# Performance work log

Measured on AMD Instinct MI355X. Metric: run time of the kernel, lower is better.

The kernel has to match this reference:

```python
import jax, jax.numpy as jnp
import numpy as np
from jax import lax

B, T, D_IN = 16, 512, 128
H_ENC, D_LAT, H_CTX, H_PRED = 512, 256, 512, 512
K_STEPS, TEMP = 12, 0.1


def setup_inputs() -> dict:
    ks = jax.random.split(jax.random.key(0), 8)
    def w(i, fi, fo):
        return jax.random.normal(ks[i], (fi, fo), jnp.float32) * (1.0 / float(np.sqrt(fi)))
    return {
        "x": jax.random.normal(ks[0], (B, T, D_IN), jnp.float32),
        "enc_w1": w(1, D_IN, H_ENC), "enc_b1": jnp.zeros((H_ENC,), jnp.float32),
        "enc_w2": w(2, H_ENC, H_ENC), "enc_b2": jnp.zeros((H_ENC,), jnp.float32),
        "enc_w3": w(3, H_ENC, D_LAT), "enc_b3": jnp.zeros((D_LAT,), jnp.float32),
        "gru_wi": w(4, D_LAT, 3 * H_CTX), "gru_bi": jnp.zeros((3 * H_CTX,), jnp.float32),
        "gru_wh": w(5, H_CTX, 3 * H_CTX), "gru_bhn": jnp.zeros((H_CTX,), jnp.float32),
        "pred_w1": w(6, H_CTX, H_PRED), "pred_b1": jnp.zeros((H_PRED,), jnp.float32),
        "pred_w2": w(7, H_PRED, D_LAT), "pred_b2": jnp.zeros((D_LAT,), jnp.float32),
    }


def _gru(z, gru_wi, gru_bi, gru_wh, gru_bhn):
    # flax GRUCell: r=sig(Wir x + bir + Whr h); u=sig(Wiz x + biz + Whz h);
    Bsz = z.shape[0]
    H = gru_wh.shape[0]
    xi = z @ gru_wi + gru_bi          # [B, T, 3H] precomputed input projections
    xi = jnp.swapaxes(xi, 0, 1)       # [T, B, 3H]

    def step(h, x_t):
        hp = h @ gru_wh               # [B, 3H]
        xr, xu, xn = jnp.split(x_t, 3, axis=-1)
        hr, hu, hn = jnp.split(hp, 3, axis=-1)
        r = jax.nn.sigmoid(xr + hr)
        u = jax.nn.sigmoid(xu + hu)
        n = jnp.tanh(xn + r * (hn + gru_bhn))
        h_new = (1.0 - u) * n + u * h
        return h_new, h_new

    h0 = jnp.zeros((Bsz, H), z.dtype)
    _, outs = lax.scan(step, h0, xi)  # [T, B, H]
    return jnp.swapaxes(outs, 0, 1)   # [B, T, H]


def reference(x, enc_w1, enc_b1, enc_w2, enc_b2, enc_w3, enc_b3,
              gru_wi, gru_bi, gru_wh, gru_bhn,
              pred_w1, pred_b1, pred_w2, pred_b2):
    # Encoder MLP
    h = jax.nn.relu(x @ enc_w1 + enc_b1)
    h = jax.nn.relu(h @ enc_w2 + enc_b2)
    z = h @ enc_w3 + enc_b3                         # [B, T, D_LAT]
    # GRU context network
    c = _gru(z, gru_wi, gru_bi, gru_wh, gru_bhn)    # [B, T, H_CTX]
    # InfoNCE loss (prediction net is identical across k, so hoist it)
    c_t = c[:, :-K_STEPS, :].reshape(-1, c.shape[-1])   # [N, H_CTX], N=B*(T-K)
    p = jax.nn.relu(c_t @ pred_w1 + pred_b1) @ pred_w2 + pred_b2
    p = p / jnp.linalg.norm(p, axis=1, keepdims=True)   # [N, D_LAT]
    total = jnp.zeros((), z.dtype)
    for k in range(1, K_STEPS + 1):
        zt = z[:, k:T - K_STEPS + k, :].reshape(-1, z.shape[-1])
        zt = zt / jnp.linalg.norm(zt, axis=1, keepdims=True)
        sim = (p @ zt.T) / TEMP                         # [N, N]
        # -mean(diag(log_softmax)) = -mean(diag(sim) - logsumexp(sim, axis=1))
        total = total + (-jnp.mean(jnp.diagonal(sim) - jax.nn.logsumexp(sim, axis=1)))
    loss = total / K_STEPS
    return z, c, loss
```

## Files before the change

### kernel.cpp

```cpp
#include <hip/hip_runtime.h>
#include <cstdint>
#include <cstddef>

typedef unsigned short u16;
typedef unsigned int   u32;
typedef unsigned long long u64;
typedef __attribute__((ext_vector_type(8))) short bf16x8;
typedef __attribute__((ext_vector_type(4))) float f32x4;
typedef __attribute__((ext_vector_type(4))) unsigned int u32x4;

typedef __attribute__((address_space(1))) const unsigned int as1c_uint;
typedef __attribute__((address_space(3))) unsigned int as3_uint;

__device__ __forceinline__ void async16(const void* g, void* l) {
  __builtin_amdgcn_global_load_lds((as1c_uint*)g, (as3_uint*)l, 16, 0, 0);
}
__device__ __forceinline__ float bf2f(u16 u) {
  return __uint_as_float(((u32)u) << 16);
}
__device__ __forceinline__ u16 f2bf(float x) {
  u32 u = __float_as_uint(x);
  u32 r = u + 0x7FFFu + ((u >> 16) & 1u);
  return (u16)(r >> 16);
}

__device__ __forceinline__ void bar_lds() {
  asm volatile("s_waitcnt lgkmcnt(0)" ::: "memory");
  __builtin_amdgcn_s_barrier();
  asm volatile("" ::: "memory");
}

__device__ __forceinline__ u32 ld_u32_ic(const void* p) {
  u32 v;
  asm volatile("global_load_dword %0, %1, off sc0 sc1\n\ts_waitcnt vmcnt(0)"
               : "=v"(v) : "v"(p) : "memory");
  return v;
}
__device__ __forceinline__ void st_u32_ic(void* p, u32 v) {
  asm volatile("global_store_dword %0, %1, off sc0 sc1" :: "v"(p), "v"(v) : "memory");
}
__device__ __forceinline__ void ld_h64_ic(const void* p, u32x4& a, u32x4& b,
                                          u32x4& c, u32x4& d) {
  asm volatile(
      "global_load_dwordx4 %0, %4, off sc0 sc1\n\t"
      "global_load_dwordx4 %1, %4, off offset:16 sc0 sc1\n\t"
      "global_load_dwordx4 %2, %4, off offset:32 sc0 sc1\n\t"
      "global_load_dwordx4 %3, %4, off offset:48 sc0 sc1\n\t"
      "s_waitcnt vmcnt(0)"
      : "=&v"(a), "=&v"(b), "=&v"(c), "=&v"(d) : "v"(p) : "memory");
}

__global__ void cvt_k(const float4* __restrict__ in, ushort4* __restrict__ out) {
  int i = blockIdx.x * 256 + threadIdx.x;
  float4 v = in[i];
  ushort4 o;
  o.x = f2bf(v.x); o.y = f2bf(v.y); o.z = f2bf(v.z); o.w = f2bf(v.w);
  out[i] = o;
}

__global__ void tr_k(const float* __restrict__ in, u16* __restrict__ out, int K, int N) {
  __shared__ u16 t[32][33];
  int bn = blockIdx.x * 32, bk = blockIdx.y * 32;
  int x = threadIdx.x, y = threadIdx.y;
#pragma unroll
  for (int i = 0; i < 32; i += 8)
    t[y + i][x] = f2bf(in[(size_t)(bk + y + i) * N + bn + x]);
  __syncthreads();
#pragma unroll
  for (int i = 0; i < 32; i += 8)
    out[(size_t)(bn + y + i) * K + bk + x] = t[x][y + i];
}

__global__ __launch_bounds__(256) void gemm_k(
    const u16* __restrict__ A, const u16* __restrict__ Bt,
    const float* __restrict__ bias, u16* __restrict__ Cbf, float* __restrict__ Cf,
    int N, int K, int act) {
  __shared__ __align__(16) u16 As[128 * 32];
  __shared__ __align__(16) u16 Bs[128 * 32];
  int tid = threadIdx.x;
  int lane = tid & 63, w = tid >> 6;
  int wm = w >> 1, wn = w & 1;
  int mm = lane & 15, kh = lane >> 4;
  int m0 = blockIdx.y * 128, n0 = blockIdx.x * 128;

  f32x4 zero = {0.f, 0.f, 0.f, 0.f};
  f32x4 acc[4][4];
#pragma unroll
  for (int i = 0; i < 4; ++i)
#pragma unroll
    for (int j = 0; j < 4; ++j) acc[i][j] = zero;

  for (int kt = 0; kt < K; kt += 32) {
#pragma unroll
    for (int it = 0; it < 2; ++it) {
      int q = tid + it * 256;
      int row = q >> 2, kc = (q & 3) * 8;
      async16(A  + (size_t)(m0 + row) * K + kt + kc, &As[q * 8]);
      async16(Bt + (size_t)(n0 + row) * K + kt + kc, &Bs[q * 8]);
    }
    __syncthreads();
    bf16x8 av[4], bv[4];
#pragma unroll
    for (int i = 0; i < 4; ++i) {
      av[i] = *(const bf16x8*)&As[(wm * 64 + i * 16 + mm) * 32 + kh * 8];
      bv[i] = *(const bf16x8*)&Bs[(wn * 64 + i * 16 + mm) * 32 + kh * 8];
    }
#pragma unroll
    for (int im = 0; im < 4; ++im)
#pragma unroll
      for (int in = 0; in < 4; ++in)
        acc[im][in] = __builtin_amdgcn_mfma_f32_16x16x32_bf16(av[im], bv[in], acc[im][in], 0, 0, 0);
    __syncthreads();
  }

#pragma unroll
  for (int im = 0; im < 4; ++im)
#pragma unroll
    for (int in = 0; in < 4; ++in)
#pragma unroll
      for (int r = 0; r < 4; ++r) {
        int gm = m0 + wm * 64 + im * 16 + kh * 4 + r;
        int gn = n0 + wn * 64 + in * 16 + mm;
        float v = acc[im][in][r] + bias[gn];
        if (act) v = fmaxf(v, 0.f);
        size_t off = (size_t)gm * N + gn;
        if (Cbf) Cbf[off] = f2bf(v);
        if (Cf)  Cf[off]  = v;
      }
}

__global__ __launch_bounds__(256) void norm_k(const u16* __restrict__ in,
                                              u16* __restrict__ out, int pack) {
  int row = blockIdx.x * 4 + (threadIdx.x >> 6);
  int lane = threadIdx.x & 63;
  ushort4 v = ((const ushort4*)(in + (size_t)row * 256))[lane];
  float a = bf2f(v.x), b = bf2f(v.y), c = bf2f(v.z), d = bf2f(v.w);
  float s = a * a + b * b + c * c + d * d;
#pragma unroll
  for (int o = 32; o; o >>= 1) s += __shfl_xor(s, o);
  float rn = rsqrtf(s);
  int orow = row;
  if (pack) {
    int bb = row >> 9, tt = row & 511;
    if (tt >= 500) return;
    orow = bb * 500 + tt;
  }
  ushort4 o4;
  o4.x = f2bf(a * rn); o4.y = f2bf(b * rn);
  o4.z = f2bf(c * rn); o4.w = f2bf(d * rn);
  *(ushort4*)(out + (size_t)orow * 256 + lane * 4) = o4;
}

#define HS 520

__global__ __launch_bounds__(512, 1) void gru_k(
    const u16* __restrict__ xi, const float* __restrict__ WH,
    const float* __restrict__ BHN, float* __restrict__ cf,
    u16* __restrict__ cbf, u16* hbuf, u32* flags) {
  __shared__ __align__(16) u16 hs[16 * HS];
  __shared__ float xis[2 * 1536];
  __shared__ float gts[1536];
  __shared__ float hnf[512];

  int tid = threadIdx.x;
  int role = blockIdx.x;
  int c0 = role * 32;

  int lane = tid & 63, w = tid >> 6;
  int mm = lane & 15, kh = lane >> 4;

  bf16x8 wf[16];
  if (w < 6) {
    int gcol = (w >> 1) * 512 + c0 + (w & 1) * 16 + mm;
    int kb = kh * 8;
#pragma unroll
    for (int kk = 0; kk < 16; ++kk) {
      bf16x8 tf;
#pragma unroll
      for (int j = 0; j < 8; ++j)
        tf[j] = (short)f2bf(WH[(size_t)(kk * 32 + kb + j) * 1536 + gcol]);
      wf[kk] = tf;
    }
  }
  int cr = tid >> 4, cj = (tid & 15) * 2;
  float bhn0 = 0.f, bhn1 = 0.f;
  if (w < 4) { bhn0 = BHN[c0 + cj]; bhn1 = BHN[c0 + cj + 1]; }

  int tt = tid - 384;
  size_t xoff[12];
  u16 xpre[12];
  if (w >= 6) {
#pragma unroll
    for (int j = 0; j < 12; ++j) {
      int v = j * 128 + tt;
      int b = v / 96, q = v - b * 96;
      int gcol = (q >> 5) * 512 + c0 + (q & 31);
      xoff[j] = (size_t)b * 512 * 1536 + gcol;
      xis[v] = bf2f(xi[xoff[j]]);
    }
#pragma unroll
    for (int j = 0; j < 12; ++j) xpre[j] = xi[xoff[j] + 1536];
  }

  for (int t = 0; t < 512; ++t) {
    if (w < 4) {
      if (t == 0) {
        for (int i = tid; i < 16 * HS; i += 256) hs[i] = 0;
      } else {
        int iter = 0;
        const u32* fl = &flags[tid & 15];
        while (ld_u32_ic(fl) < (u32)t) { if (++iter > (1 << 20)) break; }
        const u16* hb = hbuf + (size_t)(t & 1) * 8192 + (tid >> 4) * 512 + (tid & 15) * 32;
        u32x4 a, b, c, d;
        ld_h64_ic(hb, a, b, c, d);
        u32x4* dst = (u32x4*)&hs[(tid >> 4) * HS + (tid & 15) * 32];
        dst[0] = a; dst[1] = b; dst[2] = c; dst[3] = d;
      }
    } else if (w >= 6) {
      if (t > 0) {
        int v = tt * 4;
        int b = v >> 5, col = v & 31;
        size_t co = ((size_t)b * 512 + (t - 1)) * 512 + c0 + col;
        float4 o;
        o.x = hnf[v]; o.y = hnf[v + 1]; o.z = hnf[v + 2]; o.w = hnf[v + 3];
        *(float4*)&cf[co] = o;
        uint2 pk;
        pk.x = (u32)f2bf(o.x) | ((u32)f2bf(o.y) << 16);
        pk.y = (u32)f2bf(o.z) | ((u32)f2bf(o.w) << 16);
        *(uint2*)&cbf[co] = pk;
      }
      if (t < 511) {
        float* xd = &xis[((t + 1) & 1) * 1536];
#pragma unroll
        for (int j = 0; j < 12; ++j) xd[j * 128 + tt] = bf2f(xpre[j]);
      }
      if (t < 510) {
        const u16* xs = xi + (size_t)(t + 2) * 1536;
#pragma unroll
        for (int j = 0; j < 12; ++j) xpre[j] = xs[xoff[j]];
      }
    }
    bar_lds();

    if (w < 6) {
      f32x4 acc = {0.f, 0.f, 0.f, 0.f};
#pragma unroll
      for (int kk = 0; kk < 16; ++kk) {
        bf16x8 a = *(const bf16x8*)&hs[mm * HS + kk * 32 + kh * 8];
        acc = __builtin_amdgcn_mfma_f32_16x16x32_bf16(a, wf[kk], acc, 0, 0, 0);
      }
      int gc = (w >> 1) * 32 + (w & 1) * 16 + mm;
#pragma unroll
      for (int r = 0; r < 4; ++r) gts[(kh * 4 + r) * 96 + gc] = acc[r];
    }
    bar_lds();

    if (w < 4) {
      const float* xc = &xis[(t & 1) * 1536] + cr * 96;
      const float* gr_ = &gts[cr * 96];
      float hp0 = bf2f(hs[cr * HS + c0 + cj]);
      float hp1 = bf2f(hs[cr * HS + c0 + cj + 1]);
      float r0 = 1.f / (1.f + __expf(-(xc[cj] + gr_[cj])));
      float u0 = 1.f / (1.f + __expf(-(xc[32 + cj] + gr_[32 + cj])));
      float nx0 = xc[64 + cj] + r0 * (gr_[64 + cj] + bhn0);
      float n0 = 1.f - 2.f / (__expf(2.f * nx0) + 1.f);
      float h0 = (1.f - u0) * n0 + u0 * hp0;
      float r1 = 1.f / (1.f + __expf(-(xc[cj + 1] + gr_[cj + 1])));
      float u1 = 1.f / (1.f + __expf(-(xc[33 + cj] + gr_[33 + cj])));
      float nx1 = xc[65 + cj] + r1 * (gr_[65 + cj] + bhn1);
      float n1 = 1.f - 2.f / (__expf(2.f * nx1) + 1.f);
      float h1v = (1.f - u1) * n1 + u1 * hp1;
      hnf[cr * 32 + cj] = h0;
      hnf[cr * 32 + cj + 1] = h1v;
      u32 pk = (u32)f2bf(h0) | ((u32)f2bf(h1v) << 16);
      st_u32_ic(hbuf + (size_t)((t + 1) & 1) * 8192 + cr * 512 + c0 + cj, pk);
      asm volatile("s_waitcnt vmcnt(0)" ::: "memory");
    }
    bar_lds();
    if (tid == 0) st_u32_ic(&flags[role], (u32)(t + 1));
  }

  if (w >= 6) {
    int v = tt * 4;
    int b = v >> 5, col = v & 31;
    size_t co = ((size_t)b * 512 + 511) * 512 + c0 + col;
    float4 o;
    o.x = hnf[v]; o.y = hnf[v + 1]; o.z = hnf[v + 2]; o.w = hnf[v + 3];
    *(float4*)&cf[co] = o;
    uint2 pk;
    pk.x = (u32)f2bf(o.x) | ((u32)f2bf(o.y) << 16);
    pk.y = (u32)f2bf(o.z) | ((u32)f2bf(o.w) << 16);
    *(uint2*)&cbf[co] = pk;
  }
}

__global__ __launch_bounds__(256) void sgemm_k(
    const u16* __restrict__ P, const u16* __restrict__ Z,
    float* __restrict__ g, float* __restrict__ diag) {
  __shared__ __align__(16) u16 Ap[128 * 256];
  __shared__ __align__(16) u16 Bs[128 * 32];
  __shared__ float gacc[128 * 128];
  int tid = threadIdx.x;
  int lane = tid & 63, w = tid >> 6;
  int wm = w >> 1, wn = w & 1;
  int mm = lane & 15, kh = lane >> 4;
  int r0 = blockIdx.y * 128, t0 = blockIdx.x * 128;

#pragma unroll
  for (int it = 0; it < 16; ++it) {
    int q = tid + it * 256;
    int row = q >> 5, kc = (q & 31) * 8;
    async16(P + (size_t)(r0 + row) * 256 + kc, &Ap[q * 8]);
  }
  for (int i = tid; i < 128 * 128; i += 256) gacc[i] = 0.f;
  __syncthreads();

  f32x4 zero = {0.f, 0.f, 0.f, 0.f};
  for (int b = 0; b < 16; ++b) {
    int n0 = b * 512 + t0;
    f32x4 acc[4][4];
#pragma unroll
    for (int i = 0; i < 4; ++i)
#pragma unroll
      for (int j = 0; j < 4; ++j) acc[i][j] = zero;

    for (int kk = 0; kk < 8; ++kk) {
#pragma unroll
      for (int it = 0; it < 2; ++it) {
        int q = tid + it * 256;
        int row = q >> 2, kc = (q & 3) * 8;
        async16(Z + (size_t)(n0 + row) * 256 + kk * 32 + kc, &Bs[q * 8]);
      }
      __syncthreads();
      bf16x8 av[4], bv[4];
#pragma unroll
      for (int i = 0; i < 4; ++i) {
        av[i] = *(const bf16x8*)&Ap[(wm * 64 + i * 16 + mm) * 256 + kk * 32 + kh * 8];
        bv[i] = *(const bf16x8*)&Bs[(wn * 64 + i * 16 + mm) * 32 + kh * 8];
      }
#pragma unroll
      for (int im = 0; im < 4; ++im)
#pragma unroll
        for (int in = 0; in < 4; ++in)
          acc[im][in] = __builtin_amdgcn_mfma_f32_16x16x32_bf16(av[im], bv[in], acc[im][in], 0, 0, 0);
      __syncthreads();
    }
#pragma unroll
    for (int im = 0; im < 4; ++im)
#pragma unroll
      for (int in = 0; in < 4; ++in)
#pragma unroll
        for (int r = 0; r < 4; ++r) {
          int row = wm * 64 + im * 16 + kh * 4 + r;
          int col = wn * 64 + in * 16 + mm;
          float s10 = acc[im][in][r] * 10.f;
          gacc[row * 128 + col] += __expf(s10 - 10.f);
          int ig = r0 + row;
          if (ig < 8000) {
            int bi = ig / 500;
            if (bi == b) {
              int ti = ig - bi * 500;
              int dt = t0 + col - ti;
              if (dt >= 1 && dt <= 12) diag[(size_t)ig * 12 + dt - 1] = s10;
            }
          }
        }
  }
  __syncthreads();
  for (int i = tid; i < 128 * 128; i += 256) {
    int row = i >> 7, col = i & 127;
    g[(size_t)(r0 + row) * 512 + t0 + col] = gacc[i];
  }
}

__global__ __launch_bounds__(256) void win_k(const float* __restrict__ g,
                                             const float* __restrict__ diag,
                                             float* __restrict__ acc) {
  __shared__ float lo[4][16], hi[4][16];
  int w = threadIdx.x >> 6, lane = threadIdx.x & 63;
  int row = blockIdx.x * 4 + w;
  const float* gr = g + (size_t)row * 512;
  float4 a = ((const float4*)gr)[lane * 2];
  float4 b = ((const float4*)gr)[lane * 2 + 1];
  float s = a.x + a.y + a.z + a.w + b.x + b.y + b.z + b.w;
#pragma unroll
  for (int o = 32; o; o >>= 1) s += __shfl_xor(s, o);
  if (lane == 0) { lo[w][0]=a.x; lo[w][1]=a.y; lo[w][2]=a.z; lo[w][3]=a.w;
                   lo[w][4]=b.x; lo[w][5]=b.y; lo[w][6]=b.z; lo[w][7]=b.w; }
  if (lane == 1) { lo[w][8]=a.x; lo[w][9]=a.y; lo[w][10]=a.z; lo[w][11]=a.w; }
  if (lane == 62){ hi[w][0]=b.x; hi[w][1]=b.y; hi[w][2]=b.z; hi[w][3]=b.w; }
  if (lane == 63){ hi[w][4]=a.x; hi[w][5]=a.y; hi[w][6]=a.z; hi[w][7]=a.w;
                   hi[w][8]=b.x; hi[w][9]=b.y; hi[w][10]=b.z; hi[w][11]=b.w; }
  __syncthreads();
  float term = 0.f;
  if (lane < 12) {
    int k = lane + 1;
    float pre = 0.f, suf = 0.f;
#pragma unroll
    for (int j = 0; j < 12; ++j) {
      if (j < k) pre += lo[w][j];
      if (j >= k) suf += hi[w][j];
    }
    float W = s - pre - suf;
    term = diag[(size_t)row * 12 + lane] - __logf(W) - 10.f;
  }
#pragma unroll
  for (int o = 32; o; o >>= 1) term += __shfl_xor(term, o);
  if (lane == 0) atomicAdd(acc, term);
}

__global__ void fin_k(const float* acc, float* lout) {
  lout[0] = -acc[0] * (1.f / 96000.f);
}

extern "C" void kernel_launch(void* const* d_in, const int* in_sizes, int n_in,
                              void* d_out, int out_size, void* d_ws, size_t ws_size,
                              hipStream_t stream) {
  (void)in_sizes; (void)n_in; (void)out_size; (void)ws_size;
  const float* x    = (const float*)d_in[0];
  const float* ew1  = (const float*)d_in[1];
  const float* eb1  = (const float*)d_in[2];
  const float* ew2  = (const float*)d_in[3];
  const float* eb2  = (const float*)d_in[4];
  const float* ew3  = (const float*)d_in[5];
  const float* eb3  = (const float*)d_in[6];
  const float* gwi  = (const float*)d_in[7];
  const float* gbi  = (const float*)d_in[8];
  const float* gwh  = (const float*)d_in[9];
  const float* gbhn = (const float*)d_in[10];
  const float* pw1  = (const float*)d_in[11];
  const float* pb1  = (const float*)d_in[12];
  const float* pw2  = (const float*)d_in[13];
  const float* pb2  = (const float*)d_in[14];

  char* W = (char*)d_ws;
  u32*   flags = (u32*)(W + 64);
  float* lacc = (float*)(W + 2048);
  u16*   w1T  = (u16*)(W + 4096);
  u16*   w2T  = (u16*)(W + 135168);
  u16*   w3T  = (u16*)(W + 659456);
  u16*   wiT  = (u16*)(W + 921600);
  u16*   p1T  = (u16*)(W + 1708032);
  u16*   p2T  = (u16*)(W + 2232320);
  u16*   hbuf = (u16*)(W + 2494464);
  float* diag = (float*)(W + 2527232);
  u16*   zhat = (u16*)(W + 2911232);
  u16*   zbf  = (u16*)(W + 7105536);
  u16*   cbf  = (u16*)(W + 7105536);
  u16*   ppk  = (u16*)(W + 7105536);
  u16*   xi   = (u16*)(W + 15494144);
  u16*   xbf  = (u16*)(W + 15494144);
  u16*   h1   = (u16*)(W + 17591296);
  u16*   h2   = (u16*)(W + 25979904);
  float* g    = (float*)(W + 15494144);

  float* zf    = (float*)d_out;
  float* cf    = zf + 2097152;
  float* lout  = zf + 6291456;

  hipMemsetAsync(d_ws, 0, 4096, stream);

  cvt_k<<<1024, 256, 0, stream>>>((const float4*)x, (ushort4*)xbf);

  dim3 tb(32, 8);
  tr_k<<<dim3(16, 4),  tb, 0, stream>>>(ew1, w1T, 128, 512);
  tr_k<<<dim3(16, 16), tb, 0, stream>>>(ew2, w2T, 512, 512);
  tr_k<<<dim3(8, 16),  tb, 0, stream>>>(ew3, w3T, 512, 256);
  tr_k<<<dim3(48, 8),  tb, 0, stream>>>(gwi, wiT, 256, 1536);
  tr_k<<<dim3(16, 16), tb, 0, stream>>>(pw1, p1T, 512, 512);
  tr_k<<<dim3(8, 16),  tb, 0, stream>>>(pw2, p2T, 512, 256);

  gemm_k<<<dim3(4, 64),  256, 0, stream>>>(xbf,  w1T, eb1, h1,  nullptr, 512, 128, 1);
  gemm_k<<<dim3(4, 64),  256, 0, stream>>>(h1,   w2T, eb2, h2,  nullptr, 512, 512, 1);
  gemm_k<<<dim3(2, 64),  256, 0, stream>>>(h2,   w3T, eb3, zbf, zf,      256, 512, 0);
  norm_k<<<2048, 256, 0, stream>>>(zbf, zhat, 0);
  gemm_k<<<dim3(12, 64), 256, 0, stream>>>(zbf,  wiT, gbi, xi,  nullptr, 1536, 256, 0);
  gru_k<<<16, 512, 0, stream>>>(xi, gwh, gbhn, cf, cbf, hbuf, flags);
  gemm_k<<<dim3(4, 64),  256, 0, stream>>>(cbf,  p1T, pb1, h1,  nullptr, 512, 512, 1);
  gemm_k<<<dim3(2, 64),  256, 0, stream>>>(h1,   p2T, pb2, h2,  nullptr, 256, 512, 0);
  norm_k<<<2048, 256, 0, stream>>>(h2, ppk, 1);
  sgemm_k<<<dim3(4, 63), 256, 0, stream>>>(ppk, zhat, g, diag);
  win_k<<<2000, 256, 0, stream>>>(g, diag, lacc);
  fin_k<<<1, 1, 0, stream>>>(lacc, lout);
}
```

Baseline: 1.913 ms.

## Double-buffer LDS tiles in GEMM kernels and merge prep kernels into one launch

Result: no change. 1.887 ms, median of 2 (-1.3%).

```diff
diff --git a/kernel.cpp b/kernel.cpp
--- a/kernel.cpp
+++ b/kernel.cpp
@@ -50,33 +50,51 @@
       : "=&v"(a), "=&v"(b), "=&v"(c), "=&v"(d) : "v"(p) : "memory");
 }
 
-__global__ void cvt_k(const float4* __restrict__ in, ushort4* __restrict__ out) {
-  int i = blockIdx.x * 256 + threadIdx.x;
-  float4 v = in[i];
-  ushort4 o;
-  o.x = f2bf(v.x); o.y = f2bf(v.y); o.z = f2bf(v.z); o.w = f2bf(v.w);
-  out[i] = o;
-}
-
-__global__ void tr_k(const float* __restrict__ in, u16* __restrict__ out, int K, int N) {
+__global__ __launch_bounds__(256) void prep_k(
+    const float* __restrict__ x, u16* __restrict__ xbf,
+    const float* __restrict__ ew1, u16* __restrict__ w1T,
+    const float* __restrict__ ew2, u16* __restrict__ w2T,
+    const float* __restrict__ ew3, u16* __restrict__ w3T,
+    const float* __restrict__ gwi, u16* __restrict__ wiT,
+    const float* __restrict__ pw1, u16* __restrict__ p1T,
+    const float* __restrict__ pw2, u16* __restrict__ p2T) {
+  int b = blockIdx.x;
+  int tid = threadIdx.x;
+  if (b < 1024) {
+    int i = b * 256 + tid;
+    float4 v = ((const float4*)x)[i];
+    ushort4 o;
+    o.x = f2bf(v.x); o.y = f2bf(v.y); o.z = f2bf(v.z); o.w = f2bf(v.w);
+    ((ushort4*)xbf)[i] = o;
+    return;
+  }
+  b -= 1024;
+  const float* in; u16* out; int K, N, gx, idx;
+  if      (b <   64) { in = ew1; out = w1T; K = 128; N =  512; gx = 16; idx = b;        }
+  else if (b <  320) { in = ew2; out = w2T; K = 512; N =  512; gx = 16; idx = b -   64; }
+  else if (b <  448) { in = ew3; out = w3T; K = 512; N =  256; gx =  8; idx = b -  320; }
+  else if (b <  832) { in = gwi; out = wiT; K = 256; N = 1536; gx = 48; idx = b -  448; }
+  else if (b < 1088) { in = pw1; out = p1T; K = 512; N =  512; gx = 16; idx = b -  832; }
+  else               { in = pw2; out = p2T; K = 512; N =  256; gx =  8; idx = b - 1088; }
+  int bx = idx % gx, by = idx / gx;
   __shared__ u16 t[32][33];
-  int bn = blockIdx.x * 32, bk = blockIdx.y * 32;
-  int x = threadIdx.x, y = threadIdx.y;
+  int bn = bx * 32, bk = by * 32;
+  int x_ = tid & 31, y = tid >> 5;
 #pragma unroll
   for (int i = 0; i < 32; i += 8)
-    t[y + i][x] = f2bf(in[(size_t)(bk + y + i) * N + bn + x]);
+    t[y + i][x_] = f2bf(in[(size_t)(bk + y + i) * N + bn + x_]);
   __syncthreads();
 #pragma unroll
   for (int i = 0; i < 32; i += 8)
-    out[(size_t)(bn + y + i) * K + bk + x] = t[x][y + i];
+    out[(size_t)(bn + y + i) * K + bk + x_] = t[x_][y + i];
 }
 
 __global__ __launch_bounds__(256) void gemm_k(
     const u16* __restrict__ A, const u16* __restrict__ Bt,
     const float* __restrict__ bias, u16* __restrict__ Cbf, float* __restrict__ Cf,
     int N, int K, int act) {
-  __shared__ __align__(16) u16 As[128 * 32];
-  __shared__ __align__(16) u16 Bs[128 * 32];
+  __shared__ __align__(16) u16 As[2][128 * 32];
+  __shared__ __align__(16) u16 Bs[2][128 * 32];
   int tid = threadIdx.x;
   int lane = tid & 63, w = tid >> 6;
   int wm = w >> 1, wn = w & 1;
@@ -90,20 +108,30 @@
 #pragma unroll
     for (int j = 0; j < 4; ++j) acc[i][j] = zero;
 
-  for (int kt = 0; kt < K; kt += 32) {
-#pragma unroll
-    for (int it = 0; it < 2; ++it) {
-      int q = tid + it * 256;
-      int row = q >> 2, kc = (q & 3) * 8;
-      async16(A  + (size_t)(m0 + row) * K + kt + kc, &As[q * 8]);
-      async16(Bt + (size_t)(n0 + row) * K + kt + kc, &Bs[q * 8]);
-    }
-    __syncthreads();
+  int row0 = tid >> 2, kc0 = (tid & 3) * 8;
+  int row1 = (tid + 256) >> 2, kc1 = ((tid + 256) & 3) * 8;
+
+  async16(A  + (size_t)(m0 + row0) * K + kc0, &As[0][tid * 8]);
+  async16(Bt + (size_t)(n0 + row0) * K + kc0, &Bs[0][tid * 8]);
+  async16(A  + (size_t)(m0 + row1) * K + kc1, &As[0][(tid + 256) * 8]);
+  async16(Bt + (size_t)(n0 + row1) * K + kc1, &Bs[0][(tid + 256) * 8]);
+  __syncthreads();
+
+  int nk = K >> 5;
+  for (int ki = 0; ki < nk; ++ki) {
+    int cur = ki & 1, nxt = cur ^ 1;
+    if (ki + 1 < nk) {
+      int kt = (ki + 1) * 32;
+      async16(A  + (size_t)(m0 + row0) * K + kt + kc0, &As[nxt][tid * 8]);
+      async16(Bt + (size_t)(n0 + row0) * K + kt + kc0, &Bs[nxt][tid * 8]);
+      async16(A  + (size_t)(m0 + row1) * K + kt + kc1, &As[nxt][(tid + 256) * 8]);
+      async16(Bt + (size_t)(n0 + row1) * K + kt + kc1, &Bs[nxt][(tid + 256) * 8]);
+    }
     bf16x8 av[4], bv[4];
 #pragma unroll
     for (int i = 0; i < 4; ++i) {
-      av[i] = *(const bf16x8*)&As[(wm * 64 + i * 16 + mm) * 32 + kh * 8];
-      bv[i] = *(const bf16x8*)&Bs[(wn * 64 + i * 16 + mm) * 32 + kh * 8];
+      av[i] = *(const bf16x8*)&As[cur][(wm * 64 + i * 16 + mm) * 32 + kh * 8];
+      bv[i] = *(const bf16x8*)&Bs[cur][(wn * 64 + i * 16 + mm) * 32 + kh * 8];
     }
 #pragma unroll
     for (int im = 0; im < 4; ++im)
@@ -298,7 +326,7 @@
     const u16* __restrict__ P, const u16* __restrict__ Z,
     float* __restrict__ g, float* __restrict__ diag) {
   __shared__ __align__(16) u16 Ap[128 * 256];
-  __shared__ __align__(16) u16 Bs[128 * 32];
+  __shared__ __align__(16) u16 Bs[2][128 * 32];
   __shared__ float gacc[128 * 128];
   int tid = threadIdx.x;
   int lane = tid & 63, w = tid >> 6;
@@ -306,12 +334,17 @@
   int mm = lane & 15, kh = lane >> 4;
   int r0 = blockIdx.y * 128, t0 = blockIdx.x * 128;
 
+  int zrow0 = tid >> 2, zkc0 = (tid & 3) * 8;
+  int zrow1 = (tid + 256) >> 2, zkc1 = ((tid + 256) & 3) * 8;
+
 #pragma unroll
   for (int it = 0; it < 16; ++it) {
     int q = tid + it * 256;
     int row = q >> 5, kc = (q & 31) * 8;
     async16(P + (size_t)(r0 + row) * 256 + kc, &Ap[q * 8]);
   }
+  async16(Z + (size_t)(t0 + zrow0) * 256 + zkc0, &Bs[0][tid * 8]);
+  async16(Z + (size_t)(t0 + zrow1) * 256 + zkc1, &Bs[0][(tid + 256) * 8]);
   for (int i = tid; i < 128 * 128; i += 256) gacc[i] = 0.f;
   __syncthreads();
 
@@ -325,18 +358,18 @@
       for (int j = 0; j < 4; ++j) acc[i][j] = zero;
 
     for (int kk = 0; kk < 8; ++kk) {
-#pragma unroll
-      for (int it = 0; it < 2; ++it) {
-        int q = tid + it * 256;
-        int row = q >> 2, kc = (q & 3) * 8;
-        async16(Z + (size_t)(n0 + row) * 256 + kk * 32 + kc, &Bs[q * 8]);
-      }
-      __syncthreads();
+      int it = b * 8 + kk, cur = it & 1;
+      if (it + 1 < 128) {
+        int nb = (it + 1) >> 3, nkk = (it + 1) & 7;
+        int nn0 = nb * 512 + t0;
+        async16(Z + (size_t)(nn0 + zrow0) * 256 + nkk * 32 + zkc0, &Bs[cur ^ 1][tid * 8]);
+        async16(Z + (size_t)(nn0 + zrow1) * 256 + nkk * 32 + zkc1, &Bs[cur ^ 1][(tid + 256) * 8]);
+      }
       bf16x8 av[4], bv[4];
 #pragma unroll
       for (int i = 0; i < 4; ++i) {
         av[i] = *(const bf16x8*)&Ap[(wm * 64 + i * 16 + mm) * 256 + kk * 32 + kh * 8];
-        bv[i] = *(const bf16x8*)&Bs[(wn * 64 + i * 16 + mm) * 32 + kh * 8];
+        bv[i] = *(const bf16x8*)&Bs[cur][(wn * 64 + i * 16 + mm) * 32 + kh * 8];
       }
 #pragma unroll
       for (int im = 0; im < 4; ++im)
@@ -460,15 +493,8 @@
 
   hipMemsetAsync(d_ws, 0, 4096, stream);
 
-  cvt_k<<<1024, 256, 0, stream>>>((const float4*)x, (ushort4*)xbf);
-
-  dim3 tb(32, 8);
-  tr_k<<<dim3(16, 4),  tb, 0, stream>>>(ew1, w1T, 128, 512);
-  tr_k<<<dim3(16, 16), tb, 0, stream>>>(ew2, w2T, 512, 512);
-  tr_k<<<dim3(8, 16),  tb, 0, stream>>>(ew3, w3T, 512, 256);
-  tr_k<<<dim3(48, 8),  tb, 0, stream>>>(gwi, wiT, 256, 1536);
-  tr_k<<<dim3(16, 16), tb, 0, stream>>>(pw1, p1T, 512, 512);
-  tr_k<<<dim3(8, 16),  tb, 0, stream>>>(pw2, p2T, 512, 256);
+  prep_k<<<2240, 256, 0, stream>>>(x, xbf, ew1, w1T, ew2, w2T, ew3, w3T,
+                                   gwi, wiT, pw1, p1T, pw2, p2T);
 
   gemm_k<<<dim3(4, 64),  256, 0, stream>>>(xbf,  w1T, eb1, h1,  nullptr, 512, 128, 1);
   gemm_k<<<dim3(4, 64),  256, 0, stream>>>(h1,   w2T, eb2, h2,  nullptr, 512, 512, 1);
```
